# Kernel tuning notes

Measured on AMD Instinct MI355X. Metric: run time of the kernel, lower is better.

The kernel has to match this reference:

```python
import jax, jax.numpy as jnp
import numpy as np


def setup_inputs() -> dict:
    key = jax.random.key(0)
    B, T = 16, 2048
    # encoding dim must be T + 1 (1 padding row + T signal rows)
    x = jax.random.normal(key, (B, T + 1, T), dtype=jnp.float32)
    return {"x": x}


def reference(x):
    # x: [B, D, T] with D == T + 1
    B, D, T = x.shape
    pad = x[:, 0, :]                 # [B, T]  (index_select dim=1, idx [0])
    sig = x[:, 1:T + 1, :]           # [B, T, T] (index_select dim=1, idx 1..T)
    # L1 norm over encoding dim (torch.norm(signal, dim=1, p=1))
    sig_norm = jnp.sum(jnp.abs(sig), axis=1)          # [B, T]
    # 2-way softmax over (pad, norm); first column == sigmoid(pad - norm)
    w = jax.nn.sigmoid(pad - sig_norm)                # [B, T]
    pad_weighted = (w * pad)[:, None, :]              # [B, 1, T]
    # NB: torch reshapes signal to [B*T, T] row-major, so the (1 - w) gate
    # indexed by flat row i = (b, d) multiplies along the *encoding* axis.
    sig_weighted = (1.0 - w)[:, :, None] * sig        # [B, T, T]
    return jnp.concatenate([pad_weighted, sig_weighted], axis=1)  # [B, T+1, T]
```

## Files before the change

### kernel.cpp

```cpp
#include <hip/hip_runtime.h>


#define TDIM 2048
#define BDIM 16
#define COLS 32
#define NTHREADS 512

typedef float floatx4 __attribute__((ext_vector_type(4)));

__global__ __launch_bounds__(NTHREADS, 8) void pb_kernel(const float* __restrict__ x,
                                                         float* __restrict__ out) {
    const int blk    = blockIdx.x;
    const int b      = blk / (TDIM / COLS);
    const int stripe = blk % (TDIM / COLS);
    const int c0     = stripe * COLS;
    const int t      = threadIdx.x;

    const size_t planeStride = (size_t)(TDIM + 1) * TDIM;
    const float* xb  = x   + (size_t)b * planeStride;
    float*       ob  = out + (size_t)b * planeStride;
    const float* sig = xb + TDIM;

    const int li = t & 7;
    const int g  = t >> 3;
    const int colbase = c0 + 4 * li;

    float a0 = 0.f, a1 = 0.f, a2 = 0.f, a3 = 0.f;
    for (int r = g; r < TDIM; r += 64) {
        const floatx4 v = *reinterpret_cast<const floatx4*>(sig + (size_t)r * TDIM + colbase);
        a0 += fabsf(v.x); a1 += fabsf(v.y); a2 += fabsf(v.z); a3 += fabsf(v.w);
    }

    __shared__ float lds_p[64][COLS];
    lds_p[g][4 * li + 0] = a0;
    lds_p[g][4 * li + 1] = a1;
    lds_p[g][4 * li + 2] = a2;
    lds_p[g][4 * li + 3] = a3;

    __shared__ float lds_scale[COLS];
    __syncthreads();

    if (t < COLS) {
        float s = 0.f;
        #pragma unroll
        for (int gg = 0; gg < 64; ++gg) s += lds_p[gg][t];
        const float p = xb[c0 + t];
        const float w = 1.0f / (1.0f + expf(s - p));
        ob[c0 + t]    = w * p;
        lds_scale[t]  = 1.0f - w;
    }
    __syncthreads();

    for (int r = 0; r < COLS; ++r) {
        const float  sc     = lds_scale[r];
        const size_t rowoff = (size_t)(c0 + r) * TDIM;
        const floatx4* src = reinterpret_cast<const floatx4*>(sig + rowoff);
        floatx4*       dst = reinterpret_cast<floatx4*>(ob + TDIM + rowoff);
        floatx4 v = src[t];
        v.x *= sc; v.y *= sc; v.z *= sc; v.w *= sc;
        __builtin_nontemporal_store(v, dst + t);
    }
}

extern "C" void kernel_launch(void* const* d_in, const int* in_sizes, int n_in,
                              void* d_out, int out_size, void* d_ws, size_t ws_size,
                              hipStream_t stream) {
    const float* x   = (const float*)d_in[0];
    float*       out = (float*)d_out;
    const int nblocks = BDIM * (TDIM / COLS);
    pb_kernel<<<nblocks, NTHREADS, 0, stream>>>(x, out);
}
```

Baseline: 121.7 us.

## Split into coalesced column-sum kernel with atomics and separate row-scale kernel

Replaces the fused kernel with two passes. The first pass has each block read full contiguous row tiles and accumulate absolute column sums into a zeroed workspace with atomicAdd. The second pass reads those sums, computes the gate and scales row tiles, walking blocks in reverse so the most recently read tiles may still be in cache. This trades the strided 128-byte column-stripe reads for fully coalesced row reads, at the cost of a memset, an extra launch and contended global atomics.

```diff
diff --git a/kernel.cpp b/kernel.cpp
--- a/kernel.cpp
+++ b/kernel.cpp
@@ -3,62 +3,70 @@
 
 #define TDIM 2048
 #define BDIM 16
-#define COLS 32
+#define ROWS 32
 #define NTHREADS 512
 
 typedef float floatx4 __attribute__((ext_vector_type(4)));
 
-__global__ __launch_bounds__(NTHREADS, 8) void pb_kernel(const float* __restrict__ x,
-                                                         float* __restrict__ out) {
-    const int blk    = blockIdx.x;
-    const int b      = blk / (TDIM / COLS);
-    const int stripe = blk % (TDIM / COLS);
-    const int c0     = stripe * COLS;
-    const int t      = threadIdx.x;
+__global__ __launch_bounds__(NTHREADS, 8) void colsum_kernel(const float* __restrict__ x,
+                                                             float* __restrict__ ws) {
+    const int blk  = blockIdx.x;
+    const int b    = blk / (TDIM / ROWS);
+    const int tile = blk % (TDIM / ROWS);
+    const int r0   = tile * ROWS;
+    const int t    = threadIdx.x;
 
-    const size_t planeStride = (size_t)(TDIM + 1) * TDIM;
-    const float* xb  = x   + (size_t)b * planeStride;
-    float*       ob  = out + (size_t)b * planeStride;
-    const float* sig = xb + TDIM;
-
-    const int li = t & 7;
-    const int g  = t >> 3;
-    const int colbase = c0 + 4 * li;
+    const size_t plane = (size_t)(TDIM + 1) * TDIM;
+    const float* sig = x + (size_t)b * plane + TDIM;
+    const float* base = sig + (size_t)r0 * TDIM + 4 * t;
 
     float a0 = 0.f, a1 = 0.f, a2 = 0.f, a3 = 0.f;
-    for (int r = g; r < TDIM; r += 64) {
-        const floatx4 v = *reinterpret_cast<const floatx4*>(sig + (size_t)r * TDIM + colbase);
+    #pragma unroll 8
+    for (int r = 0; r < ROWS; ++r) {
+        const floatx4 v = *reinterpret_cast<const floatx4*>(base + (size_t)r * TDIM);
         a0 += fabsf(v.x); a1 += fabsf(v.y); a2 += fabsf(v.z); a3 += fabsf(v.w);
     }
 
-    __shared__ float lds_p[64][COLS];
-    lds_p[g][4 * li + 0] = a0;
-    lds_p[g][4 * li + 1] = a1;
-    lds_p[g][4 * li + 2] = a2;
-    lds_p[g][4 * li + 3] = a3;
+    float* wsb = ws + (size_t)b * TDIM + 4 * t;
+    atomicAdd(wsb + 0, a0);
+    atomicAdd(wsb + 1, a1);
+    atomicAdd(wsb + 2, a2);
+    atomicAdd(wsb + 3, a3);
+}
 
-    __shared__ float lds_scale[COLS];
-    __syncthreads();
+__global__ __launch_bounds__(NTHREADS, 8) void scale_kernel(const float* __restrict__ x,
+                                                            const float* __restrict__ ws,
+                                                            float* __restrict__ out) {
+    const int nb   = BDIM * (TDIM / ROWS);
+    const int blk  = nb - 1 - blockIdx.x;
+    const int b    = blk / (TDIM / ROWS);
+    const int tile = blk % (TDIM / ROWS);
+    const int r0   = tile * ROWS;
+    const int t    = threadIdx.x;
 
-    if (t < COLS) {
-        float s = 0.f;
-        #pragma unroll
-        for (int gg = 0; gg < 64; ++gg) s += lds_p[gg][t];
-        const float p = xb[c0 + t];
+    const size_t plane = (size_t)(TDIM + 1) * TDIM;
+    const float* xb  = x   + (size_t)b * plane;
+    float*       ob  = out + (size_t)b * plane;
+    const float* sig = xb + TDIM;
+
+    __shared__ float lds_scale[ROWS];
+    if (t < ROWS) {
+        const float s = ws[(size_t)b * TDIM + r0 + t];
+        const float p = xb[r0 + t];
         const float w = 1.0f / (1.0f + expf(s - p));
-        ob[c0 + t]    = w * p;
+        ob[r0 + t]    = w * p;
         lds_scale[t]  = 1.0f - w;
     }
     __syncthreads();
 
-    for (int r = 0; r < COLS; ++r) {
-        const float  sc     = lds_scale[r];
-        const size_t rowoff = (size_t)(c0 + r) * TDIM;
-        const floatx4* src = reinterpret_cast<const floatx4*>(sig + rowoff);
-        floatx4*       dst = reinterpret_cast<floatx4*>(ob + TDIM + rowoff);
-        floatx4 v = src[t];
+    const float* srcb = sig + (size_t)r0 * TDIM;
+    float*       dstb = ob + TDIM + (size_t)r0 * TDIM;
+    #pragma unroll 4
+    for (int r = 0; r < ROWS; ++r) {
+        floatx4 v = *reinterpret_cast<const floatx4*>(srcb + (size_t)r * TDIM + 4 * t);
+        const float sc = lds_scale[r];
         v.x *= sc; v.y *= sc; v.z *= sc; v.w *= sc;
-        __builtin_nontemporal_store(v, dst + t);
+        __builtin_nontemporal_store(v, reinterpret_cast<floatx4*>(dstb + (size_t)r * TDIM + 4 * t));
     }
 }
 
@@ -67,6 +75,11 @@
                               hipStream_t stream) {
     const float* x   = (const float*)d_in[0];
     float*       out = (float*)d_out;
-    const int nblocks = BDIM * (TDIM / COLS);
-    pb_kernel<<<nblocks, NTHREADS, 0, stream>>>(x, out);
+    float*       ws  = (float*)d_ws;
+
+    hipMemsetAsync(ws, 0, (size_t)BDIM * TDIM * sizeof(float), stream);
+
+    const int nblocks = BDIM * (TDIM / ROWS);
+    colsum_kernel<<<nblocks, NTHREADS, 0, stream>>>(x, ws);
+    scale_kernel <<<nblocks, NTHREADS, 0, stream>>>(x, ws, out);
 }
```

After: 147.9 us. 1.22x slower.
